# Performance work log

Hardware: AMD Instinct MI355X
Metric: run time of the kernel (lower is better)

Reference implementation:

```python
import jax, jax.numpy as jnp
import numpy as np

B = 2048        # batch of observations (vmapped agent)
OBS_DIM = 4096
N_GVFS = 4096
INPUTS_PER_GVF = 16
HID_PER_GVF = 8
N_ACTIONS = 18
TOTAL_FEAT = OBS_DIM + HID_PER_GVF * N_GVFS  # 36864


def setup_inputs() -> dict:
    key = jax.random.key(0)
    k_obs, k_gvf, k_q, k_idx = jax.random.split(key, 4)
    observation = jax.random.normal(k_obs, (B, OBS_DIM), dtype=jnp.float32)
    # per-GVF shared hidden layer weights (no bias): (n_gvfs, hidden, inputs)
    gvf_W = jax.random.normal(k_gvf, (N_GVFS, HID_PER_GVF, INPUTS_PER_GVF), dtype=jnp.float32) * 0.05
    # bias-free Q head over concatenated features: (n_actions, total_feat)
    q_W = jax.random.normal(k_q, (N_ACTIONS, TOTAL_FEAT), dtype=jnp.float32) * 0.02
    gvf_input_idxs = jax.random.randint(k_idx, (N_GVFS, INPUTS_PER_GVF), 0, OBS_DIM)
    return {"observation": observation, "gvf_W": gvf_W, "q_W": q_W,
            "gvf_input_idxs": gvf_input_idxs}


def reference(observation, gvf_W, q_W, gvf_input_idxs):
    # get_gvf_inputs: fancy gather per GVF -> (B, n_gvfs, inputs_per_gvf)
    gvf_inputs = observation[:, gvf_input_idxs]
    # compute_shared_representation of each tiny GVF net: relu(W @ x), vmapped
    gvf_feats = jax.nn.relu(jnp.einsum('bgi,ghi->bgh', gvf_inputs, gvf_W))
    # compute_all_features: concat obs with flattened GVF features
    features = jnp.concatenate(
        [observation, gvf_feats.reshape(observation.shape[0], -1)], axis=-1)
    # output_layer.action_values: bias-free linear Q-head
    q_values = jnp.einsum('bf,af->ba', features, q_W)  # (B, n_actions)
    return q_values
```

## Files before the change

### kernel.cpp

```cpp
#include <hip/hip_runtime.h>

#define B_SZ 2048
#define OBS_DIM 4096
#define N_GVFS 4096
#define IPG 16
#define HPG 8
#define N_ACT 18
#define TOTAL_FEAT (OBS_DIM + HPG * N_GVFS)

#define BT 8
#define NTHREADS 512
#define CHUNK 128
#define NCHUNK (N_GVFS / CHUNK)

#define WS_WT 0u
#define WS_Q 1048576u
#define WS_IDX 2228224u
#define WS_NEED 2359296u

__device__ __forceinline__ unsigned short f32_bf16_rne(float f) {
    unsigned int u = __float_as_uint(f);
    u += 0x7FFFu + ((u >> 16) & 1u);
    return (unsigned short)(u >> 16);
}
__device__ __forceinline__ float bf_lo(unsigned int p) { return __uint_as_float(p << 16); }
__device__ __forceinline__ float bf_hi(unsigned int p) { return __uint_as_float(p & 0xFFFF0000u); }

__device__ __forceinline__ void gll16(const void* g, void* l) {
    __builtin_amdgcn_global_load_lds(
        (const __attribute__((address_space(1))) unsigned int*)g,
        (__attribute__((address_space(3))) unsigned int*)l, 16, 0, 0);
}
__device__ __forceinline__ void gll4(const void* g, void* l) {
    __builtin_amdgcn_global_load_lds(
        (const __attribute__((address_space(1))) unsigned int*)g,
        (__attribute__((address_space(3))) unsigned int*)l, 4, 0, 0);
}

__global__ __launch_bounds__(256) void pack_wt_kernel(const float* __restrict__ W,
                                                      unsigned short* __restrict__ dst) {
    const int id = blockIdx.x * 256 + threadIdx.x;
    const int i = id >> 12, g = id & 4095;
    unsigned int p[4];
#pragma unroll
    for (int hp = 0; hp < 4; ++hp) {
        const float a = W[g * 128 + (2 * hp) * 16 + i];
        const float b = W[g * 128 + (2 * hp + 1) * 16 + i];
        p[hp] = (unsigned int)f32_bf16_rne(a) | ((unsigned int)f32_bf16_rne(b) << 16);
    }
    *(uint4*)(dst + (size_t)(i * 4096 + g) * 8) = make_uint4(p[0], p[1], p[2], p[3]);
}

__global__ __launch_bounds__(256) void pack_q_kernel(const float* __restrict__ qW,
                                                     unsigned short* __restrict__ dst) {
    const int id = blockIdx.x * 256 + threadIdx.x;
    const int a = id >> 12, g = id & 4095;
    const float* src = qW + (size_t)a * TOTAL_FEAT + OBS_DIM + (size_t)g * 8;
    const float4 f0 = *(const float4*)(src);
    const float4 f1 = *(const float4*)(src + 4);
    unsigned int p0 = (unsigned int)f32_bf16_rne(f0.x) | ((unsigned int)f32_bf16_rne(f0.y) << 16);
    unsigned int p1 = (unsigned int)f32_bf16_rne(f0.z) | ((unsigned int)f32_bf16_rne(f0.w) << 16);
    unsigned int p2 = (unsigned int)f32_bf16_rne(f1.x) | ((unsigned int)f32_bf16_rne(f1.y) << 16);
    unsigned int p3 = (unsigned int)f32_bf16_rne(f1.z) | ((unsigned int)f32_bf16_rne(f1.w) << 16);
    *(uint4*)(dst + (size_t)(a * 4096 + g) * 8) = make_uint4(p0, p1, p2, p3);
}

__global__ __launch_bounds__(256) void pack_idx_kernel(const int* __restrict__ gidx,
                                                       unsigned short* __restrict__ dst) {
    const int id = blockIdx.x * 256 + threadIdx.x;
    const int i = id >> 12, g = id & 4095;
    dst[(size_t)i * 4096 + g] = (unsigned short)gidx[g * 16 + i];
}

__global__ __launch_bounds__(NTHREADS)
void fused_kernel(const float* __restrict__ obs,
                  const float* __restrict__ qW,
                  const unsigned char* __restrict__ ws,
                  float* __restrict__ out)
{
    __shared__ __align__(16) unsigned short obs_t[OBS_DIM * BT];
    __shared__ __align__(16) unsigned short wt_s[IPG * CHUNK * HPG];
    __shared__ __align__(16) unsigned short q_s[N_ACT * CHUNK * HPG];
    __shared__ __align__(16) unsigned short idx_s[IPG * CHUNK];
    __shared__ float red2[8][2][N_ACT];

    const int tid  = threadIdx.x;
    const int b0   = blockIdx.x * BT;
    const int lane = tid & 63;
    const int wv   = tid >> 6;
    const int h    = tid >> 7;
    const int s    = tid & (CHUNK - 1);

    for (int m = 0; m < 16; ++m) {
        const int id  = tid + NTHREADS * m;
        const int row = id & 7;
        const int j4  = id >> 3;
        const float4 v4 = *(const float4*)(obs + (size_t)(b0 + row) * OBS_DIM + j4 * 4);
        const float vv[4] = {v4.x, v4.y, v4.z, v4.w};
        char* base = (char*)obs_t + row * 2;
#pragma unroll
        for (int c = 0; c < 4; ++c)
            *(unsigned short*)(base + (size_t)(j4 * 4 + c) * 16) = f32_bf16_rne(vv[c]);
    }

    float qacc[2][N_ACT];
#pragma unroll
    for (int r = 0; r < 2; ++r)
#pragma unroll
        for (int a = 0; a < N_ACT; ++a) qacc[r][a] = 0.f;

    const unsigned char* wsWt  = ws + WS_WT;
    const unsigned char* wsQ   = ws + WS_Q;
    const unsigned char* wsIdx = ws + WS_IDX;

#pragma unroll 1
    for (int k = 0; k < NCHUNK; ++k) {
        __syncthreads();

        for (int p = wv; p < 50; p += 8) {
            if (p < 16) {
                const unsigned char* src = wsWt + (size_t)p * (N_GVFS * HPG * 2)
                                                + (size_t)k * (CHUNK * HPG * 2);
                char* dst = (char*)wt_s + p * (CHUNK * HPG * 2);
                gll16(src + lane * 16, dst);
                gll16(src + 1024 + lane * 16, dst + 1024);
            } else if (p < 34) {
                const int a = p - 16;
                const unsigned char* src = wsQ + (size_t)a * (N_GVFS * HPG * 2)
                                               + (size_t)k * (CHUNK * HPG * 2);
                char* dst = (char*)q_s + a * (CHUNK * HPG * 2);
                gll16(src + lane * 16, dst);
                gll16(src + 1024 + lane * 16, dst + 1024);
            } else {
                const int i = p - 34;
                const unsigned char* src = wsIdx + (size_t)i * (N_GVFS * 2)
                                                 + (size_t)k * (CHUNK * 2);
                char* dst = (char*)idx_s + i * (CHUNK * 2);
                gll4(src + lane * 4, dst);
            }
        }
        __syncthreads();

        int jv[IPG];
#pragma unroll
        for (int i = 0; i < IPG; ++i) jv[i] = idx_s[i * CHUNK + s];

        float v0[HPG], v1[HPG];
#pragma unroll
        for (int hh = 0; hh < HPG; ++hh) { v0[hh] = 0.f; v1[hh] = 0.f; }

#pragma unroll
        for (int i = 0; i < IPG; ++i) {
            const unsigned int xp = *(const unsigned int*)((const char*)obs_t + jv[i] * 16 + h * 4);
            const float x0 = bf_lo(xp), x1 = bf_hi(xp);
            const uint4 wp = *(const uint4*)((const char*)wt_s + (size_t)(i * CHUNK + s) * 16);
            float wr[HPG];
            wr[0] = bf_lo(wp.x); wr[1] = bf_hi(wp.x);
            wr[2] = bf_lo(wp.y); wr[3] = bf_hi(wp.y);
            wr[4] = bf_lo(wp.z); wr[5] = bf_hi(wp.z);
            wr[6] = bf_lo(wp.w); wr[7] = bf_hi(wp.w);
#pragma unroll
            for (int hh = 0; hh < HPG; ++hh) {
                v0[hh] = fmaf(x0, wr[hh], v0[hh]);
                v1[hh] = fmaf(x1, wr[hh], v1[hh]);
            }
        }
#pragma unroll
        for (int hh = 0; hh < HPG; ++hh) {
            v0[hh] = fmaxf(v0[hh], 0.f);
            v1[hh] = fmaxf(v1[hh], 0.f);
        }

#pragma unroll
        for (int a = 0; a < N_ACT; ++a) {
            const uint4 qp = *(const uint4*)((const char*)q_s + (size_t)(a * CHUNK + s) * 16);
            float qr[HPG];
            qr[0] = bf_lo(qp.x); qr[1] = bf_hi(qp.x);
            qr[2] = bf_lo(qp.y); qr[3] = bf_hi(qp.y);
            qr[4] = bf_lo(qp.z); qr[5] = bf_hi(qp.z);
            qr[6] = bf_lo(qp.w); qr[7] = bf_hi(qp.w);
            float a0 = qacc[0][a], a1 = qacc[1][a];
#pragma unroll
            for (int hh = 0; hh < HPG; ++hh) {
                a0 = fmaf(v0[hh], qr[hh], a0);
                a1 = fmaf(v1[hh], qr[hh], a1);
            }
            qacc[0][a] = a0; qacc[1][a] = a1;
        }
    }

#pragma unroll 1
    for (int jj = 0; jj < OBS_DIM / (CHUNK * 4); ++jj) {
        const int j = (jj * CHUNK + s) * 4;
        const float4 o0 = *(const float4*)(obs + (size_t)(b0 + 2 * h) * OBS_DIM + j);
        const float4 o1 = *(const float4*)(obs + (size_t)(b0 + 2 * h + 1) * OBS_DIM + j);
#pragma unroll
        for (int a = 0; a < N_ACT; ++a) {
            const float4 q4 = *(const float4*)(qW + (size_t)a * TOTAL_FEAT + j);
            qacc[0][a] = fmaf(o0.x, q4.x, fmaf(o0.y, q4.y, fmaf(o0.z, q4.z, fmaf(o0.w, q4.w, qacc[0][a]))));
            qacc[1][a] = fmaf(o1.x, q4.x, fmaf(o1.y, q4.y, fmaf(o1.z, q4.z, fmaf(o1.w, q4.w, qacc[1][a]))));
        }
    }

#pragma unroll
    for (int r = 0; r < 2; ++r)
#pragma unroll
        for (int a = 0; a < N_ACT; ++a) {
            float t = qacc[r][a];
#pragma unroll
            for (int m2 = 1; m2 < 64; m2 <<= 1) t += __shfl_xor(t, m2, 64);
            if (lane == 0) red2[wv][r][a] = t;
        }
    __syncthreads();
    if (tid < BT * N_ACT) {
        const int row = tid / N_ACT, a = tid % N_ACT;
        const int w0 = (row >> 1) * 2, r = row & 1;
        out[(size_t)(b0 + row) * N_ACT + a] = red2[w0][r][a] + red2[w0 + 1][r][a];
    }
}

__global__ __launch_bounds__(256)
void fallback_kernel(const float* __restrict__ obs, const float* __restrict__ W,
                     const float* __restrict__ qW, const int* __restrict__ gidx,
                     float* __restrict__ out)
{
    const int b = blockIdx.x, t = threadIdx.x;
    float acc[N_ACT];
#pragma unroll
    for (int a = 0; a < N_ACT; ++a) acc[a] = 0.f;
    for (int g = t; g < N_GVFS; g += 256) {
        float v[HPG];
#pragma unroll
        for (int hh = 0; hh < HPG; ++hh) v[hh] = 0.f;
        for (int i = 0; i < IPG; ++i) {
            const float x = obs[(size_t)b * OBS_DIM + gidx[g * 16 + i]];
#pragma unroll
            for (int hh = 0; hh < HPG; ++hh)
                v[hh] = fmaf(x, W[g * 128 + hh * 16 + i], v[hh]);
        }
#pragma unroll
        for (int hh = 0; hh < HPG; ++hh) v[hh] = fmaxf(v[hh], 0.f);
#pragma unroll
        for (int a = 0; a < N_ACT; ++a) {
            float t2 = 0.f;
#pragma unroll
            for (int hh = 0; hh < HPG; ++hh)
                t2 = fmaf(v[hh], qW[(size_t)a * TOTAL_FEAT + OBS_DIM + g * 8 + hh], t2);
            acc[a] += t2;
        }
    }
    for (int j = t; j < OBS_DIM; j += 256) {
        const float x = obs[(size_t)b * OBS_DIM + j];
#pragma unroll
        for (int a = 0; a < N_ACT; ++a)
            acc[a] = fmaf(x, qW[(size_t)a * TOTAL_FEAT + j], acc[a]);
    }
    __shared__ float rr[4][N_ACT];
    const int lane = t & 63, w = t >> 6;
#pragma unroll
    for (int a = 0; a < N_ACT; ++a) {
        float x = acc[a];
#pragma unroll
        for (int m = 1; m < 64; m <<= 1) x += __shfl_xor(x, m, 64);
        if (lane == 0) rr[w][a] = x;
    }
    __syncthreads();
    if (t < N_ACT)
        out[(size_t)b * N_ACT + t] = rr[0][t] + rr[1][t] + rr[2][t] + rr[3][t];
}

extern "C" void kernel_launch(void* const* d_in, const int* in_sizes, int n_in,
                              void* d_out, int out_size, void* d_ws, size_t ws_size,
                              hipStream_t stream) {
    const float* obs  = (const float*)d_in[0];
    const float* gvfW = (const float*)d_in[1];
    const float* qW   = (const float*)d_in[2];
    const int*   gidx = (const int*)d_in[3];
    float* out = (float*)d_out;

    if (ws_size >= WS_NEED) {
        unsigned char* ws = (unsigned char*)d_ws;
        pack_wt_kernel<<<dim3(256), dim3(256), 0, stream>>>(gvfW, (unsigned short*)(ws + WS_WT));
        pack_q_kernel<<<dim3(288), dim3(256), 0, stream>>>(qW, (unsigned short*)(ws + WS_Q));
        pack_idx_kernel<<<dim3(256), dim3(256), 0, stream>>>(gidx, (unsigned short*)(ws + WS_IDX));
        fused_kernel<<<dim3(B_SZ / BT), dim3(NTHREADS), 0, stream>>>(obs, qW, ws, out);
    } else {
        fallback_kernel<<<dim3(B_SZ), dim3(256), 0, stream>>>(obs, gvfW, qW, gidx, out);
    }
}
```

Measured before the change: 224.2 us.

## Switch GVF and Q-head math to packed fp16 dot2 with swizzled LDS layout

Replaces the bf16 unpack-and-FMA inner loops with packed fp16 values and v_dot2 instructions, halving the FMA count and removing the bf16-to-f32 unpack ALU work. Observations are stored in LDS as fp16 pairs with an XOR swizzle, and the precomputed index encodes the swizzle to reduce bank conflicts. The three pack kernels are merged into one launch. fp16 has less range than bf16 and conversion uses round-toward-zero, which could affect accuracy. The LDS footprint grows to about 140KB per block.

New measurement: 193.4 us. -13.7%, faster.

```diff
diff --git a/kernel.cpp b/kernel.cpp
--- a/kernel.cpp
+++ b/kernel.cpp
@@ -18,13 +18,34 @@
 #define WS_IDX 2228224u
 #define WS_NEED 2359296u
 
-__device__ __forceinline__ unsigned short f32_bf16_rne(float f) {
-    unsigned int u = __float_as_uint(f);
-    u += 0x7FFFu + ((u >> 16) & 1u);
-    return (unsigned short)(u >> 16);
-}
-__device__ __forceinline__ float bf_lo(unsigned int p) { return __uint_as_float(p << 16); }
-__device__ __forceinline__ float bf_hi(unsigned int p) { return __uint_as_float(p & 0xFFFF0000u); }
+typedef unsigned int u32;
+typedef unsigned short u16;
+typedef __attribute__((ext_vector_type(2))) __fp16 h2;
+union U32H2 { u32 u; h2 h; };
+
+__device__ __forceinline__ u32 pk_f16(float a, float b) {
+    U32H2 t; t.h = __builtin_amdgcn_cvt_pkrtz(a, b); return t.u;
+}
+
+#if __has_builtin(__builtin_amdgcn_fdot2)
+__device__ __forceinline__ float fdot2(u32 a, u32 b, float c) {
+    U32H2 x, y; x.u = a; y.u = b;
+    return __builtin_amdgcn_fdot2(x.h, y.h, c, false);
+}
+#else
+__device__ __forceinline__ float fdot2(u32 a, u32 b, float c) {
+    U32H2 x, y; x.u = a; y.u = b;
+    return fmaf((float)x.h.x, (float)y.h.x, fmaf((float)x.h.y, (float)y.h.y, c));
+}
+#endif
+
+#if __has_builtin(__builtin_amdgcn_perm)
+__device__ __forceinline__ u32 lo_pair(u32 A, u32 B) { return __builtin_amdgcn_perm(B, A, 0x05040100u); }
+__device__ __forceinline__ u32 hi_pair(u32 A, u32 B) { return __builtin_amdgcn_perm(B, A, 0x07060302u); }
+#else
+__device__ __forceinline__ u32 lo_pair(u32 A, u32 B) { return (A & 0xFFFFu) | (B << 16); }
+__device__ __forceinline__ u32 hi_pair(u32 A, u32 B) { return (A >> 16) | (B & 0xFFFF0000u); }
+#endif
 
 __device__ __forceinline__ void gll16(const void* g, void* l) {
     __builtin_amdgcn_global_load_lds(
@@ -37,39 +58,41 @@
         (__attribute__((address_space(3))) unsigned int*)l, 4, 0, 0);
 }
 
-__global__ __launch_bounds__(256) void pack_wt_kernel(const float* __restrict__ W,
-                                                      unsigned short* __restrict__ dst) {
-    const int id = blockIdx.x * 256 + threadIdx.x;
-    const int i = id >> 12, g = id & 4095;
-    unsigned int p[4];
-#pragma unroll
-    for (int hp = 0; hp < 4; ++hp) {
-        const float a = W[g * 128 + (2 * hp) * 16 + i];
-        const float b = W[g * 128 + (2 * hp + 1) * 16 + i];
-        p[hp] = (unsigned int)f32_bf16_rne(a) | ((unsigned int)f32_bf16_rne(b) << 16);
-    }
-    *(uint4*)(dst + (size_t)(i * 4096 + g) * 8) = make_uint4(p[0], p[1], p[2], p[3]);
-}
-
-__global__ __launch_bounds__(256) void pack_q_kernel(const float* __restrict__ qW,
-                                                     unsigned short* __restrict__ dst) {
-    const int id = blockIdx.x * 256 + threadIdx.x;
-    const int a = id >> 12, g = id & 4095;
-    const float* src = qW + (size_t)a * TOTAL_FEAT + OBS_DIM + (size_t)g * 8;
-    const float4 f0 = *(const float4*)(src);
-    const float4 f1 = *(const float4*)(src + 4);
-    unsigned int p0 = (unsigned int)f32_bf16_rne(f0.x) | ((unsigned int)f32_bf16_rne(f0.y) << 16);
-    unsigned int p1 = (unsigned int)f32_bf16_rne(f0.z) | ((unsigned int)f32_bf16_rne(f0.w) << 16);
-    unsigned int p2 = (unsigned int)f32_bf16_rne(f1.x) | ((unsigned int)f32_bf16_rne(f1.y) << 16);
-    unsigned int p3 = (unsigned int)f32_bf16_rne(f1.z) | ((unsigned int)f32_bf16_rne(f1.w) << 16);
-    *(uint4*)(dst + (size_t)(a * 4096 + g) * 8) = make_uint4(p0, p1, p2, p3);
-}
-
-__global__ __launch_bounds__(256) void pack_idx_kernel(const int* __restrict__ gidx,
-                                                       unsigned short* __restrict__ dst) {
-    const int id = blockIdx.x * 256 + threadIdx.x;
-    const int i = id >> 12, g = id & 4095;
-    dst[(size_t)i * 4096 + g] = (unsigned short)gidx[g * 16 + i];
+__global__ __launch_bounds__(256)
+void pack_all_kernel(const float* __restrict__ W, const float* __restrict__ qW,
+                     const int* __restrict__ gidx, unsigned char* __restrict__ ws) {
+    const int bid = blockIdx.x, t = threadIdx.x;
+    if (bid < 128) {
+        const int id = bid * 256 + t;
+        const int g = id >> 3, hh = id & 7;
+        const float* src = W + (size_t)g * 128 + hh * 16;
+        float w[16];
+#pragma unroll
+        for (int q4 = 0; q4 < 4; ++q4) {
+            const float4 f = *(const float4*)(src + q4 * 4);
+            w[q4 * 4 + 0] = f.x; w[q4 * 4 + 1] = f.y; w[q4 * 4 + 2] = f.z; w[q4 * 4 + 3] = f.w;
+        }
+        u32* dst = (u32*)(ws + WS_WT);
+#pragma unroll
+        for (int pp = 0; pp < 8; ++pp) {
+            const int pe = pp * 2 + (hh >> 2);
+            dst[(size_t)(pe * 4096 + g) * 4 + (hh & 3)] = pk_f16(w[2 * pp], w[2 * pp + 1]);
+        }
+    } else if (bid < 416) {
+        const int id = (bid - 128) * 256 + t;
+        const int a = id >> 12, g = id & 4095;
+        const float* src = qW + (size_t)a * TOTAL_FEAT + OBS_DIM + (size_t)g * 8;
+        const float4 f0 = *(const float4*)(src);
+        const float4 f1 = *(const float4*)(src + 4);
+        u32* dst = (u32*)(ws + WS_Q) + (size_t)(a * 4096 + g) * 4;
+        dst[0] = pk_f16(f0.x, f0.y); dst[1] = pk_f16(f0.z, f0.w);
+        dst[2] = pk_f16(f1.x, f1.y); dst[3] = pk_f16(f1.z, f1.w);
+    } else {
+        const int id = (bid - 416) * 256 + t;
+        const int i = id >> 12, g = id & 4095;
+        const u32 j = (u32)gidx[g * 16 + i];
+        ((u16*)(ws + WS_IDX))[(size_t)i * 4096 + g] = (u16)((j << 4) | ((j >> 3) & 3));
+    }
 }
 
 __global__ __launch_bounds__(NTHREADS)
@@ -78,11 +101,12 @@
                   const unsigned char* __restrict__ ws,
                   float* __restrict__ out)
 {
-    __shared__ __align__(16) unsigned short obs_t[OBS_DIM * BT];
-    __shared__ __align__(16) unsigned short wt_s[IPG * CHUNK * HPG];
-    __shared__ __align__(16) unsigned short q_s[N_ACT * CHUNK * HPG];
-    __shared__ __align__(16) unsigned short idx_s[IPG * CHUNK];
-    __shared__ float red2[8][2][N_ACT];
+    __shared__ __align__(16) unsigned char lds[65536 + 32768 + 36864 + 4096 + 1152];
+    unsigned char* const obs_c = lds;
+    unsigned char* const wt_c  = lds + 65536;
+    unsigned char* const q_c   = lds + 98304;
+    unsigned char* const idx_c = lds + 135168;
+    float* const red2          = (float*)(lds + 139264);
 
     const int tid  = threadIdx.x;
     const int b0   = blockIdx.x * BT;
@@ -91,16 +115,13 @@
     const int h    = tid >> 7;
     const int s    = tid & (CHUNK - 1);
 
-    for (int m = 0; m < 16; ++m) {
-        const int id  = tid + NTHREADS * m;
-        const int row = id & 7;
-        const int j4  = id >> 3;
-        const float4 v4 = *(const float4*)(obs + (size_t)(b0 + row) * OBS_DIM + j4 * 4);
-        const float vv[4] = {v4.x, v4.y, v4.z, v4.w};
-        char* base = (char*)obs_t + row * 2;
-#pragma unroll
-        for (int c = 0; c < 4; ++c)
-            *(unsigned short*)(base + (size_t)(j4 * 4 + c) * 16) = f32_bf16_rne(vv[c]);
+    for (int m = 0; m < 32; ++m) {
+        const int id = tid + NTHREADS * m;
+        const int j = id & 4095, p = id >> 12;
+        const float a = obs[(size_t)(b0 + 2 * p) * OBS_DIM + j];
+        const float b = obs[(size_t)(b0 + 2 * p + 1) * OBS_DIM + j];
+        const int w = p ^ ((j >> 3) & 3);
+        *(u32*)(obs_c + j * 16 + w * 4) = pk_f16(a, b);
     }
 
     float qacc[2][N_ACT];
@@ -119,72 +140,68 @@
 
         for (int p = wv; p < 50; p += 8) {
             if (p < 16) {
-                const unsigned char* src = wsWt + (size_t)p * (N_GVFS * HPG * 2)
-                                                + (size_t)k * (CHUNK * HPG * 2);
-                char* dst = (char*)wt_s + p * (CHUNK * HPG * 2);
+                const unsigned char* src = wsWt + ((size_t)p * 4096 + k * CHUNK) * 16;
+                unsigned char* dst = wt_c + p * 2048;
                 gll16(src + lane * 16, dst);
                 gll16(src + 1024 + lane * 16, dst + 1024);
             } else if (p < 34) {
                 const int a = p - 16;
-                const unsigned char* src = wsQ + (size_t)a * (N_GVFS * HPG * 2)
-                                               + (size_t)k * (CHUNK * HPG * 2);
-                char* dst = (char*)q_s + a * (CHUNK * HPG * 2);
+                const unsigned char* src = wsQ + ((size_t)a * 4096 + k * CHUNK) * 16;
+                unsigned char* dst = q_c + a * 2048;
                 gll16(src + lane * 16, dst);
                 gll16(src + 1024 + lane * 16, dst + 1024);
             } else {
                 const int i = p - 34;
-                const unsigned char* src = wsIdx + (size_t)i * (N_GVFS * 2)
-                                                 + (size_t)k * (CHUNK * 2);
-                char* dst = (char*)idx_s + i * (CHUNK * 2);
-                gll4(src + lane * 4, dst);
+                const unsigned char* src = wsIdx + ((size_t)i * 4096 + k * CHUNK) * 2;
+                gll4(src + lane * 4, idx_c + i * 256);
             }
         }
         __syncthreads();
 
-        int jv[IPG];
-#pragma unroll
-        for (int i = 0; i < IPG; ++i) jv[i] = idx_s[i * CHUNK + s];
+        int ga[IPG];
+#pragma unroll
+        for (int i = 0; i < IPG; ++i) {
+            const u32 t16 = *(const u16*)(idx_c + i * 256 + s * 2);
+            ga[i] = (int)(t16 & 0xFFF0u) + ((((u32)h ^ t16) & 3u) << 2);
+        }
 
         float v0[HPG], v1[HPG];
 #pragma unroll
         for (int hh = 0; hh < HPG; ++hh) { v0[hh] = 0.f; v1[hh] = 0.f; }
 
 #pragma unroll
-        for (int i = 0; i < IPG; ++i) {
-            const unsigned int xp = *(const unsigned int*)((const char*)obs_t + jv[i] * 16 + h * 4);
-            const float x0 = bf_lo(xp), x1 = bf_hi(xp);
-            const uint4 wp = *(const uint4*)((const char*)wt_s + (size_t)(i * CHUNK + s) * 16);
-            float wr[HPG];
-            wr[0] = bf_lo(wp.x); wr[1] = bf_hi(wp.x);
-            wr[2] = bf_lo(wp.y); wr[3] = bf_hi(wp.y);
-            wr[4] = bf_lo(wp.z); wr[5] = bf_hi(wp.z);
-            wr[6] = bf_lo(wp.w); wr[7] = bf_hi(wp.w);
-#pragma unroll
-            for (int hh = 0; hh < HPG; ++hh) {
-                v0[hh] = fmaf(x0, wr[hh], v0[hh]);
-                v1[hh] = fmaf(x1, wr[hh], v1[hh]);
-            }
-        }
-#pragma unroll
-        for (int hh = 0; hh < HPG; ++hh) {
-            v0[hh] = fmaxf(v0[hh], 0.f);
-            v1[hh] = fmaxf(v1[hh], 0.f);
+        for (int pp = 0; pp < 8; ++pp) {
+            const u32 xA = *(const u32*)(obs_c + ga[2 * pp]);
+            const u32 xB = *(const u32*)(obs_c + ga[2 * pp + 1]);
+            const u32 x0 = lo_pair(xA, xB);
+            const u32 x1 = hi_pair(xA, xB);
+            const uint4 wA = *(const uint4*)(wt_c + ((pp * 2 + 0) * CHUNK + s) * 16);
+            const uint4 wB = *(const uint4*)(wt_c + ((pp * 2 + 1) * CHUNK + s) * 16);
+            v0[0] = fdot2(x0, wA.x, v0[0]); v1[0] = fdot2(x1, wA.x, v1[0]);
+            v0[1] = fdot2(x0, wA.y, v0[1]); v1[1] = fdot2(x1, wA.y, v1[1]);
+            v0[2] = fdot2(x0, wA.z, v0[2]); v1[2] = fdot2(x1, wA.z, v1[2]);
+            v0[3] = fdot2(x0, wA.w, v0[3]); v1[3] = fdot2(x1, wA.w, v1[3]);
+            v0[4] = fdot2(x0, wB.x, v0[4]); v1[4] = fdot2(x1, wB.x, v1[4]);
+            v0[5] = fdot2(x0, wB.y, v0[5]); v1[5] = fdot2(x1, wB.y, v1[5]);
+            v0[6] = fdot2(x0, wB.z, v0[6]); v1[6] = fdot2(x1, wB.z, v1[6]);
+            v0[7] = fdot2(x0, wB.w, v0[7]); v1[7] = fdot2(x1, wB.w, v1[7]);
+        }
+
+        u32 vp0[4], vp1[4];
+#pragma unroll
+        for (int hp = 0; hp < 4; ++hp) {
+            vp0[hp] = pk_f16(fmaxf(v0[2 * hp], 0.f), fmaxf(v0[2 * hp + 1], 0.f));
+            vp1[hp] = pk_f16(fmaxf(v1[2 * hp], 0.f), fmaxf(v1[2 * hp + 1], 0.f));
         }
 
 #pragma unroll
         for (int a = 0; a < N_ACT; ++a) {
-            const uint4 qp = *(const uint4*)((const char*)q_s + (size_t)(a * CHUNK + s) * 16);
-            float qr[HPG];
-            qr[0] = bf_lo(qp.x); qr[1] = bf_hi(qp.x);
-            qr[2] = bf_lo(qp.y); qr[3] = bf_hi(qp.y);
-            qr[4] = bf_lo(qp.z); qr[5] = bf_hi(qp.z);
-            qr[6] = bf_lo(qp.w); qr[7] = bf_hi(qp.w);
+            const uint4 qp = *(const uint4*)(q_c + (a * CHUNK + s) * 16);
             float a0 = qacc[0][a], a1 = qacc[1][a];
-#pragma unroll
-            for (int hh = 0; hh < HPG; ++hh) {
-                a0 = fmaf(v0[hh], qr[hh], a0);
-                a1 = fmaf(v1[hh], qr[hh], a1);
-            }
+            a0 = fdot2(vp0[0], qp.x, a0); a1 = fdot2(vp1[0], qp.x, a1);
+            a0 = fdot2(vp0[1], qp.y, a0); a1 = fdot2(vp1[1], qp.y, a1);
+            a0 = fdot2(vp0[2], qp.z, a0); a1 = fdot2(vp1[2], qp.z, a1);
+            a0 = fdot2(vp0[3], qp.w, a0); a1 = fdot2(vp1[3], qp.w, a1);
             qacc[0][a] = a0; qacc[1][a] = a1;
         }
     }
@@ -209,13 +226,14 @@
             float t = qacc[r][a];
 #pragma unroll
             for (int m2 = 1; m2 < 64; m2 <<= 1) t += __shfl_xor(t, m2, 64);
-            if (lane == 0) red2[wv][r][a] = t;
+            if (lane == 0) red2[(wv * 2 + r) * N_ACT + a] = t;
         }
     __syncthreads();
     if (tid < BT * N_ACT) {
         const int row = tid / N_ACT, a = tid % N_ACT;
         const int w0 = (row >> 1) * 2, r = row & 1;
-        out[(size_t)(b0 + row) * N_ACT + a] = red2[w0][r][a] + red2[w0 + 1][r][a];
+        out[(size_t)(b0 + row) * N_ACT + a] =
+            red2[(w0 * 2 + r) * N_ACT + a] + red2[((w0 + 1) * 2 + r) * N_ACT + a];
     }
 }
 
@@ -280,9 +298,7 @@
 
     if (ws_size >= WS_NEED) {
         unsigned char* ws = (unsigned char*)d_ws;
-        pack_wt_kernel<<<dim3(256), dim3(256), 0, stream>>>(gvfW, (unsigned short*)(ws + WS_WT));
-        pack_q_kernel<<<dim3(288), dim3(256), 0, stream>>>(qW, (unsigned short*)(ws + WS_Q));
-        pack_idx_kernel<<<dim3(256), dim3(256), 0, stream>>>(gidx, (unsigned short*)(ws + WS_IDX));
+        pack_all_kernel<<<dim3(672), dim3(256), 0, stream>>>(gvfW, qW, gidx, ws);
         fused_kernel<<<dim3(B_SZ / BT), dim3(NTHREADS), 0, stream>>>(obs, qW, ws, out);
     } else {
         fallback_kernel<<<dim3(B_SZ), dim3(256), 0, stream>>>(obs, gvfW, qW, gidx, out);
```
